# Kernel optimization log

Measured on AMD Instinct MI355X. Metric: run time of the kernel, lower is better.

## Reference

```python
import jax, jax.numpy as jnp
import numpy as np

B, S, D, H, DFF = 4, 2048, 1024, 16, 4096
DK = D // H
EPS = 1e-9


def setup_inputs() -> dict:
    key = jax.random.key(0)
    ks = jax.random.split(key, 12)
    s = lambda k, shape, scale: jax.random.normal(k, shape, dtype=jnp.float32) * scale
    return {
        "x": s(ks[0], (B, S, D), 1.0),
        "mask": jnp.ones((B, 1, 1, S), dtype=jnp.int32),
        # Linear weights stored torch-style [out, in]
        "wq": s(ks[1], (D, D), D ** -0.5),
        "wk": s(ks[2], (D, D), D ** -0.5),
        "wv": s(ks[3], (D, D), D ** -0.5),
        "wo": s(ks[4], (D, D), D ** -0.5),
        "w1": s(ks[5], (DFF, D), D ** -0.5),
        "b1": jnp.zeros((DFF,), jnp.float32),
        "w2": s(ks[6], (D, DFF), DFF ** -0.5),
        "b2": jnp.zeros((D,), jnp.float32),
        "g1": jnp.ones((D,), jnp.float32),
        "be1": jnp.zeros((D,), jnp.float32),
        "g2": jnp.ones((D,), jnp.float32),
        "be2": jnp.zeros((D,), jnp.float32),
    }


def _layernorm(x, gamma, beta):
    # Matches AddAndNorm: torch.std uses Bessel correction (ddof=1)
    mean = jnp.mean(x, axis=-1, keepdims=True)
    var = jnp.sum((x - mean) ** 2, axis=-1, keepdims=True) / (x.shape[-1] - 1)
    return gamma * (x - mean) / jnp.sqrt(var + EPS) + beta


def _mha(x, mask, wq, wk, wv, wo):
    b, s, d = x.shape
    def proj(w):  # [b,s,d] @ [d,d]^T -> heads [b,h,s,dk]
        return (x @ w.T).reshape(b, s, H, DK).transpose(0, 2, 1, 3)
    q, k, v = proj(wq), proj(wk), proj(wv)
    scores = jnp.einsum("bhqd,bhkd->bhqk", q, k) / jnp.sqrt(jnp.float32(DK))
    scores = jnp.where(mask == 0, jnp.float32(-1e9), scores)
    attn = jax.nn.softmax(scores, axis=-1)
    out = jnp.einsum("bhqk,bhkd->bhqd", attn, v)
    out = out.transpose(0, 2, 1, 3).reshape(b, s, d)
    return out @ wo.T


def reference(x, mask, wq, wk, wv, wo, w1, b1, w2, b2, g1, be1, g2, be2):
    # Residual 1: x + MHA(LN(x))  (dropout = 0)
    h1 = x + _mha(_layernorm(x, g1, be1), mask, wq, wk, wv, wo)
    # Residual 2: h1 + FFN(LN(h1))
    z = _layernorm(h1, g2, be2)
    ffn = jax.nn.relu(z @ w1.T + b1) @ w2.T + b2
    return h1 + ffn
```

## Files before the change

kernel.cpp:

```cpp
#include <hip/hip_runtime.h>
#include <hip/hip_bf16.h>
#include <cstdint>
#include <cstddef>

typedef __attribute__((ext_vector_type(8))) short short8;
typedef __attribute__((ext_vector_type(4))) float floatx4;
typedef __attribute__((ext_vector_type(4))) unsigned short ushort4e;

#define B_   4
#define S_   2048
#define D_   1024
#define H_   16
#define DK_  64
#define DFF_ 4096
#define MTOT (B_ * S_)
#define QKVLD 3072

__device__ __forceinline__ float bf2f(unsigned short u) {
    union { unsigned int i; float f; } v; v.i = ((unsigned int)u) << 16; return v.f;
}
__device__ __forceinline__ unsigned short f2bf(float f) {
    union { float f; unsigned int i; } v; v.f = f;
    unsigned int u = v.i;
    u += 0x7fffu + ((u >> 16) & 1u);
    return (unsigned short)(u >> 16);
}
__device__ __forceinline__ void async_cp16(const void* g, void* l) {
    __builtin_amdgcn_global_load_lds(
        (const __attribute__((address_space(1))) unsigned int*)g,
        (__attribute__((address_space(3))) unsigned int*)l,
        16, 0, 0);
}

__global__ void dtype_probe(const unsigned short* __restrict__ x, int* flag) {
    __shared__ float red[4];
    const int tid = threadIdx.x;
    float mx = 0.f;
    #pragma unroll
    for (int i = 0; i < 16; i++) {
        float v = fabsf(bf2f(x[tid * 16 + i]));
        if (v != v) v = 1e30f;
        mx = fmaxf(mx, v);
    }
    #pragma unroll
    for (int off = 32; off > 0; off >>= 1) mx = fmaxf(mx, __shfl_down(mx, off));
    if ((tid & 63) == 0) red[tid >> 6] = mx;
    __syncthreads();
    if (tid == 0) {
        float m = fmaxf(fmaxf(red[0], red[1]), fmaxf(red[2], red[3]));
        *flag = (m > 50.f) ? 1 : 0;
    }
}

__device__ __forceinline__ void cvt8(const void* src, unsigned short* dst, int i, int fl) {
    if (fl) {
        const floatx4* s = (const floatx4*)src;
        floatx4 a = s[i * 2], b = s[i * 2 + 1];
        short8 o;
        o[0] = (short)f2bf(a[0]); o[1] = (short)f2bf(a[1]);
        o[2] = (short)f2bf(a[2]); o[3] = (short)f2bf(a[3]);
        o[4] = (short)f2bf(b[0]); o[5] = (short)f2bf(b[1]);
        o[6] = (short)f2bf(b[2]); o[7] = (short)f2bf(b[3]);
        ((short8*)dst)[i] = o;
    } else {
        ((short8*)dst)[i] = ((const short8*)src)[i];
    }
}

__global__ void cvt_kernel(const void* __restrict__ src,
                           unsigned short* __restrict__ dst,
                           int n8, const int* __restrict__ flag) {
    const int i = blockIdx.x * 256 + threadIdx.x;
    if (i >= n8) return;
    cvt8(src, dst, i, *flag);
}

__global__ void cvt4_kernel(const void* s0, const void* s1, const void* s2, const void* s3,
                            unsigned short* __restrict__ dst,
                            const int* __restrict__ flag) {
    const int t = blockIdx.x >> 9;
    const int i = (blockIdx.x & 511) * 256 + threadIdx.x;
    const void* s = (t == 0) ? s0 : (t == 1) ? s1 : (t == 2) ? s2 : s3;
    cvt8(s, dst + (size_t)t * (D_ * D_), i, *flag);
}

__global__ void cvt_small(const void* b1, const void* b2, const void* g1,
                          const void* be1, const void* g2, const void* be2,
                          unsigned short* db1, unsigned short* db2, unsigned short* dg1,
                          unsigned short* dbe1, unsigned short* dg2, unsigned short* dbe2,
                          const int* __restrict__ flag) {
    const int fl = *flag;
    for (int i = threadIdx.x; i < 1152; i += 256) {
        if (i < 512)       cvt8(b1,  db1,  i,        fl);
        else if (i < 640)  cvt8(b2,  db2,  i - 512,  fl);
        else if (i < 768)  cvt8(g1,  dg1,  i - 640,  fl);
        else if (i < 896)  cvt8(be1, dbe1, i - 768,  fl);
        else if (i < 1024) cvt8(g2,  dg2,  i - 896,  fl);
        else               cvt8(be2, dbe2, i - 1024, fl);
    }
}

#define BM 128
#define BN 128
#define BK 64

template<int RELU, int HAS_BIAS, int RES_MODE, int OUT_MODE>
__global__ __launch_bounds__(256)
void gemm_bt(const unsigned short* __restrict__ A, int lda,
             const unsigned short* __restrict__ W, int ldw,
             const unsigned short* __restrict__ bias,
             const void* resid,
             void* out,
             int M, int N, int K,
             const int* __restrict__ flagp)
{
    __shared__ unsigned short As[BM * BK];
    __shared__ unsigned short Bs[BN * BK];

    const int tid  = threadIdx.x;
    const int lane = tid & 63;
    const int wave = tid >> 6;
    const int wm = wave >> 1;
    const int wn = wave & 1;
    const int lr = lane & 15;
    const int lq = lane >> 4;

    const int nwg     = gridDim.x * gridDim.y;
    const int flat    = blockIdx.y * gridDim.x + blockIdx.x;
    const int logical = (flat & 7) * (nwg >> 3) + (flat >> 3);
    const int m0 = (logical / gridDim.x) * BM;
    const int n0 = (logical % gridDim.x) * BN;

    int fl = 1;
    if (RES_MODE == 3 || OUT_MODE == 2) fl = *flagp;

    floatx4 acc[4][4];
    #pragma unroll
    for (int i = 0; i < 4; i++)
        #pragma unroll
        for (int j = 0; j < 4; j++)
            acc[i][j] = (floatx4){0.f, 0.f, 0.f, 0.f};

    const int lrow = lane >> 3;
    const int swz  = ((lane & 7) ^ lrow) * 8;
    const int rx   = lr & 7;
    const int p0   = ((lq)     ^ rx) * 8;
    const int p1   = ((4 + lq) ^ rx) * 8;

    for (int k0 = 0; k0 < K; k0 += BK) {
        #pragma unroll
        for (int t = 0; t < 4; t++) {
            const int row = wave * 32 + t * 8;
            async_cp16(A + (size_t)(m0 + row + lrow) * lda + k0 + swz, &As[row * BK]);
            async_cp16(W + (size_t)(n0 + row + lrow) * ldw + k0 + swz, &Bs[row * BK]);
        }
        __syncthreads();
        #pragma unroll
        for (int kk = 0; kk < 2; kk++) {
            const int pos = kk ? p1 : p0;
            short8 af[4], bfr[4];
            #pragma unroll
            for (int i = 0; i < 4; i++) {
                af[i]  = *(const short8*)(&As[(wm * 64 + i * 16 + lr) * BK + pos]);
                bfr[i] = *(const short8*)(&Bs[(wn * 64 + i * 16 + lr) * BK + pos]);
            }
            #pragma unroll
            for (int i = 0; i < 4; i++)
                #pragma unroll
                for (int j = 0; j < 4; j++)
                    acc[i][j] = __builtin_amdgcn_mfma_f32_16x16x32_bf16(
                                    af[i], bfr[j], acc[i][j], 0, 0, 0);
        }
        __syncthreads();
    }

    #pragma unroll
    for (int i = 0; i < 4; i++) {
        #pragma unroll
        for (int j = 0; j < 4; j++) {
            const int col = n0 + wn * 64 + j * 16 + lr;
            const float bv = HAS_BIAS ? bf2f(bias[col]) : 0.f;
            #pragma unroll
            for (int r = 0; r < 4; r++) {
                const int row = m0 + wm * 64 + i * 16 + lq * 4 + r;
                const size_t idx = (size_t)row * N + col;
                float vvv = acc[i][j][r] + bv;
                if (RES_MODE == 1) vvv += bf2f(((const unsigned short*)resid)[idx]);
                if (RES_MODE == 2) vvv += ((const float*)resid)[idx];
                if (RES_MODE == 3) vvv += fl ? ((const float*)resid)[idx]
                                             : bf2f(((const unsigned short*)resid)[idx]);
                if (RELU) vvv = fmaxf(vvv, 0.f);
                if (OUT_MODE == 1)      ((float*)out)[idx] = vvv;
                else if (OUT_MODE == 0) ((unsigned short*)out)[idx] = f2bf(vvv);
                else { if (fl) ((float*)out)[idx] = vvv;
                       else    ((unsigned short*)out)[idx] = f2bf(vvv); }
            }
        }
    }
}

#define GBM 256
#define GBN 256
#define GBK 64

__device__ __forceinline__ void gbar() {
    asm volatile("" ::: "memory");
    __builtin_amdgcn_s_barrier();
    asm volatile("" ::: "memory");
}

template<int RELU, int HAS_BIAS>
__global__ __launch_bounds__(512, 2)
void gemm256_bt(const unsigned short* __restrict__ A, int lda,
                const unsigned short* __restrict__ W, int ldw,
                const unsigned short* __restrict__ bias,
                unsigned short* __restrict__ out,
                int M, int N, int K)
{
    __shared__ unsigned short As[2][GBM * GBK];
    __shared__ unsigned short Bs[2][GBN * GBK];

    const int tid  = threadIdx.x;
    const int lane = tid & 63;
    const int wave = tid >> 6;
    const int wm   = wave >> 2;
    const int wn   = wave & 3;
    const int lr   = lane & 15;
    const int lq   = lane >> 4;

    const int nwg     = gridDim.x * gridDim.y;
    const int flat    = blockIdx.y * gridDim.x + blockIdx.x;
    const int logical = (flat & 7) * (nwg >> 3) + (flat >> 3);
    const int m0 = (logical / gridDim.x) * GBM;
    const int n0 = (logical % gridDim.x) * GBN;

    const int lrow = lane >> 3;
    const int schk = ((lane & 7) ^ lrow) * 8;
    const int rx   = lr & 7;
    const int fp0  = ((lq)     ^ rx) * 8;
    const int fp1  = ((4 + lq) ^ rx) * 8;

    floatx4 acc[8][4];
    #pragma unroll
    for (int i = 0; i < 8; i++)
        #pragma unroll
        for (int j = 0; j < 4; j++)
            acc[i][j] = (floatx4){0.f, 0.f, 0.f, 0.f};

    const int nkt = K / GBK;

    #pragma unroll
    for (int g = 0; g < 4; g++) {
        async_cp16(A + (size_t)(m0 + g * 64 + wave * 8 + lrow) * lda + schk,
                   &As[0][g * 4096 + wave * 512]);
        async_cp16(W + (size_t)(n0 + g * 64 + wave * 8 + lrow) * ldw + schk,
                   &Bs[0][g * 4096 + wave * 512]);
    }
    asm volatile("s_waitcnt vmcnt(0)" ::: "memory");
    __syncthreads();

    for (int t = 0; t < nkt; ++t) {
        const int cur   = t & 1;
        const int knext = (t + 1) * GBK;
        const bool more = (t + 1 < nkt);
        short8 bfr[4][2];

        #pragma unroll
        for (int p = 0; p < 4; ++p) {
            short8 af[2][2];
            #pragma unroll
            for (int ii = 0; ii < 2; ii++)
                #pragma unroll
                for (int kk = 0; kk < 2; kk++)
                    af[ii][kk] = *(const short8*)
                        &As[cur][(wm * 128 + p * 32 + ii * 16 + lr) * GBK + (kk ? fp1 : fp0)];
            if (p == 0) {
                #pragma unroll
                for (int j = 0; j < 4; j++)
                    #pragma unroll
                    for (int kk = 0; kk < 2; kk++)
                        bfr[j][kk] = *(const short8*)
                            &Bs[cur][(wn * 64 + j * 16 + lr) * GBK + (kk ? fp1 : fp0)];
                if (more) {
                    #pragma unroll
                    for (int g = 0; g < 4; g++)
                        async_cp16(A + (size_t)(m0 + g * 64 + wave * 8 + lrow) * lda + knext + schk,
                                   &As[cur ^ 1][g * 4096 + wave * 512]);
                }
            }
            if (p == 1 && more) {
                #pragma unroll
                for (int g = 0; g < 4; g++)
                    async_cp16(W + (size_t)(n0 + g * 64 + wave * 8 + lrow) * ldw + knext + schk,
                               &Bs[cur ^ 1][g * 4096 + wave * 512]);
            }
            if (p == 3) asm volatile("s_waitcnt vmcnt(0)" ::: "memory");
            gbar();
            __builtin_amdgcn_s_setprio(1);
            #pragma unroll
            for (int kk = 0; kk < 2; kk++)
                #pragma unroll
                for (int ii = 0; ii < 2; ii++)
                    #pragma unroll
                    for (int j = 0; j < 4; j++)
                        acc[p * 2 + ii][j] = __builtin_amdgcn_mfma_f32_16x16x32_bf16(
                                                 af[ii][kk], bfr[j][kk],
                                                 acc[p * 2 + ii][j], 0, 0, 0);
            __builtin_amdgcn_s_setprio(0);
            gbar();
        }
    }

    #pragma unroll
    for (int i = 0; i < 8; i++) {
        #pragma unroll
        for (int j = 0; j < 4; j++) {
            const int col = n0 + wn * 64 + j * 16 + lr;
            const float bv = HAS_BIAS ? bf2f(bias[col]) : 0.f;
            #pragma unroll
            for (int r = 0; r < 4; r++) {
                const int row = m0 + wm * 128 + i * 16 + lq * 4 + r;
                float vvv = acc[i][j][r] + bv;
                if (RELU) vvv = fmaxf(vvv, 0.f);
                out[(size_t)row * N + col] = f2bf(vvv);
            }
        }
    }
}

template<int IN_MODE>
__global__ __launch_bounds__(256)
void ln_kernel(const void* __restrict__ Xv,
               const unsigned short* __restrict__ g,
               const unsigned short* __restrict__ be,
               unsigned short* __restrict__ out,
               const int* __restrict__ flagp)
{
    const int row = blockIdx.x;
    const int tid = threadIdx.x;
    int fl = 1;
    if (IN_MODE == 2) fl = *flagp;
    float x4[4];
    if (IN_MODE == 1 || fl) {
        const float* X = (const float*)Xv + (size_t)row * D_ + tid * 4;
        floatx4 t = *(const floatx4*)X;
        x4[0] = t[0]; x4[1] = t[1]; x4[2] = t[2]; x4[3] = t[3];
    } else {
        const unsigned short* X = (const unsigned short*)Xv + (size_t)row * D_ + tid * 4;
        ushort4e u = *(const ushort4e*)X;
        #pragma unroll
        for (int i = 0; i < 4; i++) x4[i] = bf2f(u[i]);
    }
    float s1 = x4[0] + x4[1] + x4[2] + x4[3];
    float s2 = x4[0]*x4[0] + x4[1]*x4[1] + x4[2]*x4[2] + x4[3]*x4[3];
    #pragma unroll
    for (int off = 32; off > 0; off >>= 1) {
        s1 += __shfl_down(s1, off);
        s2 += __shfl_down(s2, off);
    }
    __shared__ float r1[4], r2[4];
    const int wv = tid >> 6;
    if ((tid & 63) == 0) { r1[wv] = s1; r2[wv] = s2; }
    __syncthreads();
    s1 = r1[0] + r1[1] + r1[2] + r1[3];
    s2 = r2[0] + r2[1] + r2[2] + r2[3];
    const float mean = s1 * (1.0f / D_);
    const float var  = (s2 - (float)D_ * mean * mean) * (1.0f / (D_ - 1));
    const float rstd = rsqrtf(var + 1e-9f);

    ushort4e o4;
    #pragma unroll
    for (int i = 0; i < 4; i++) {
        const float gv = bf2f(g[tid * 4 + i]);
        const float bv = bf2f(be[tid * 4 + i]);
        o4[i] = f2bf(gv * (x4[i] - mean) * rstd + bv);
    }
    *(ushort4e*)(out + (size_t)row * D_ + tid * 4) = o4;
}

__global__ __launch_bounds__(256)
void vtrans(const unsigned short* __restrict__ V, int ldv,
            unsigned short* __restrict__ Vt)
{
    __shared__ unsigned short t[64 * 72];
    const int tid = threadIdx.x;
    const int kt  = blockIdx.x * 64;
    const int bh  = blockIdx.y;
    const int b   = bh >> 4, h = bh & 15;
    const int r   = tid >> 2;
    const int c4  = (tid & 3) * 16;
    const unsigned short* vp = V + (size_t)(b * S_ + kt + r) * ldv + h * DK_ + c4;
    *(short8*)&t[r * 72 + c4]     = *(const short8*)vp;
    *(short8*)&t[r * 72 + c4 + 8] = *(const short8*)(vp + 8);
    __syncthreads();
    short8 o0, o1;
    #pragma unroll
    for (int e = 0; e < 8; e++) {
        o0[e] = (short)t[(c4 + e) * 72 + r];
        o1[e] = (short)t[(c4 + 8 + e) * 72 + r];
    }
    unsigned short* op = Vt + ((size_t)bh * DK_ + r) * S_ + kt + c4;
    *(short8*)op       = o0;
    *(short8*)(op + 8) = o1;
}

#define ATK   64
#define KS_LD 64
#define PS_LD 72
#define NT_   (S_ / ATK)

__global__ __launch_bounds__(256)
void attn_mfma(const unsigned short* __restrict__ QKV,
               const unsigned short* __restrict__ Vt,
               const int* __restrict__ mask,
               unsigned short* __restrict__ ctx)
{
    __shared__ unsigned short Ks[ATK * KS_LD];
    __shared__ unsigned short Vts[DK_ * KS_LD];
    __shared__ unsigned short Ps[4][32 * PS_LD];
    __shared__ float maskadd[ATK];

    const int tid  = threadIdx.x;
    const int lane = tid & 63;
    const int w    = tid >> 6;
    const int c    = lane & 15;
    const int qd   = lane >> 4;

    const int flat    = blockIdx.y * gridDim.x + blockIdx.x;
    const int logical = (flat & 7) * 64 + (flat >> 3);
    const int bh   = logical >> 3;
    const int b    = bh >> 4;
    const int h    = bh & 15;
    const int qb   = (logical & 7) * 256 + w * 32;

    const int lrow = lane >> 3;
    const int swz  = ((lane & 7) ^ lrow) * 8;
    const int cx   = c & 7;

    short8 onesf;
    #pragma unroll
    for (int e = 0; e < 8; e++) onesf[e] = (short)0x3F80;

    const float QS = 0.18033688f;
    short8 qf[2][2][2];
    #pragma unroll
    for (int qh = 0; qh < 2; qh++)
        #pragma unroll
        for (int jq = 0; jq < 2; jq++)
            #pragma unroll
            for (int kk = 0; kk < 2; kk++) {
                const unsigned short* qp =
                    QKV + (size_t)(b * S_ + qb + qh * 128 + jq * 16 + c) * QKVLD
                        + h * DK_ + kk * 32 + qd * 8;
                short8 t = *(const short8*)qp;
                short8 o;
                #pragma unroll
                for (int e = 0; e < 8; e++)
                    o[e] = (short)f2bf(bf2f((unsigned short)t[e]) * QS);
                qf[qh][jq][kk] = o;
            }

    floatx4 acc_o[2][2][4];
    floatx4 acc_l[2][2];
    #pragma unroll
    for (int qh = 0; qh < 2; qh++) {
        #pragma unroll
        for (int iq = 0; iq < 2; iq++) {
            acc_l[qh][iq] = (floatx4){0.f, 0.f, 0.f, 0.f};
            #pragma unroll
            for (int jd = 0; jd < 4; jd++)
                acc_o[qh][iq][jd] = (floatx4){0.f, 0.f, 0.f, 0.f};
        }
    }

    for (int kt = 0; kt < S_; kt += ATK) {
        {
            const unsigned short* kbase =
                QKV + 1024 + (size_t)(b * S_ + kt + w * 16) * QKVLD + h * DK_;
            const unsigned short* vbase =
                Vt + ((size_t)bh * DK_ + w * 16) * S_ + kt;
            #pragma unroll
            for (int t = 0; t < 2; t++) {
                async_cp16(kbase + (size_t)(t * 8 + lrow) * QKVLD + swz,
                           &Ks[(w * 16 + t * 8) * KS_LD]);
                async_cp16(vbase + (size_t)(t * 8 + lrow) * S_ + swz,
                           &Vts[(w * 16 + t * 8) * KS_LD]);
            }
            if (tid < ATK) maskadd[tid] = (mask[b * S_ + kt + tid] == 0) ? -1e9f : 0.f;
        }
        __syncthreads();

        #pragma unroll
        for (int qh = 0; qh < 2; qh++) {
            floatx4 acc_s[4][2];
            #pragma unroll
            for (int i = 0; i < 4; i++)
                #pragma unroll
                for (int jq = 0; jq < 2; jq++)
                    acc_s[i][jq] = (floatx4){0.f, 0.f, 0.f, 0.f};
            #pragma unroll
            for (int kk = 0; kk < 2; kk++) {
                const int pos = ((kk * 4 + qd) ^ cx) * 8;
                short8 kf[4];
                #pragma unroll
                for (int i = 0; i < 4; i++)
                    kf[i] = *(const short8*)&Ks[(i * 16 + c) * KS_LD + pos];
                __builtin_amdgcn_s_setprio(1);
                #pragma unroll
                for (int i = 0; i < 4; i++)
                    #pragma unroll
                    for (int jq = 0; jq < 2; jq++)
                        acc_s[i][jq] = __builtin_amdgcn_mfma_f32_16x16x32_bf16(
                                           kf[i], qf[qh][jq][kk], acc_s[i][jq], 0, 0, 0);
                __builtin_amdgcn_s_setprio(0);
            }

            floatx4 madd[4];
            #pragma unroll
            for (int i = 0; i < 4; i++)
                madd[i] = *(const floatx4*)&maskadd[i * 16 + qd * 4];

            #pragma unroll
            for (int jq = 0; jq < 2; jq++) {
                #pragma unroll
                for (int i = 0; i < 4; i++) {
                    floatx4 p;
                    #pragma unroll
                    for (int r = 0; r < 4; r++)
                        p[r] = __builtin_amdgcn_exp2f(acc_s[i][jq][r] + madd[i][r]);
                    unsigned int w0, w1;
                    asm("v_cvt_pk_bf16_f32 %0, %1, %2" : "=v"(w0) : "v"(p[0]), "v"(p[1]));
                    asm("v_cvt_pk_bf16_f32 %0, %1, %2" : "=v"(w1) : "v"(p[2]), "v"(p[3]));
                    uint2 pk; pk.x = w0; pk.y = w1;
                    *(uint2*)&Ps[w][(jq * 16 + c) * PS_LD + i * 16 + qd * 4] = pk;
                }
            }

            #pragma unroll
            for (int kk = 0; kk < 2; kk++) {
                const int pos = ((kk * 4 + qd) ^ cx) * 8;
                short8 pf[2], vf[4];
                #pragma unroll
                for (int iq = 0; iq < 2; iq++)
                    pf[iq] = *(const short8*)&Ps[w][(iq * 16 + c) * PS_LD + kk * 32 + qd * 8];
                #pragma unroll
                for (int jd = 0; jd < 4; jd++)
                    vf[jd] = *(const short8*)&Vts[(jd * 16 + c) * KS_LD + pos];
                __builtin_amdgcn_s_setprio(1);
                #pragma unroll
                for (int iq = 0; iq < 2; iq++) {
                    #pragma unroll
                    for (int jd = 0; jd < 4; jd++)
                        acc_o[qh][iq][jd] = __builtin_amdgcn_mfma_f32_16x16x32_bf16(
                                                pf[iq], vf[jd], acc_o[qh][iq][jd], 0, 0, 0);
                    acc_l[qh][iq] = __builtin_amdgcn_mfma_f32_16x16x32_bf16(
                                        pf[iq], onesf, acc_l[qh][iq], 0, 0, 0);
                }
                __builtin_amdgcn_s_setprio(0);
            }
        }
        __syncthreads();
    }

    #pragma unroll
    for (int qh = 0; qh < 2; qh++)
        #pragma unroll
        for (int iq = 0; iq < 2; iq++) {
            floatx4 inv;
            #pragma unroll
            for (int r = 0; r < 4; r++) inv[r] = 1.f / acc_l[qh][iq][r];
            #pragma unroll
            for (int jd = 0; jd < 4; jd++)
                #pragma unroll
                for (int r = 0; r < 4; r++) {
                    const int row = qb + qh * 128 + iq * 16 + qd * 4 + r;
                    const int col = h * DK_ + jd * 16 + c;
                    ctx[(size_t)(b * S_ + row) * D_ + col] =
                        f2bf(acc_o[qh][iq][jd][r] * inv[r]);
                }
        }
}

extern "C" void kernel_launch(void* const* d_in, const int* in_sizes, int n_in,
                              void* d_out, int out_size, void* d_ws, size_t ws_size,
                              hipStream_t stream)
{
    const void* x_raw  = d_in[0];
    const int*  mask   = (const int*)d_in[1];
    const void* wq_raw = d_in[2];
    const void* wk_raw = d_in[3];
    const void* wv_raw = d_in[4];
    const void* wo_raw = d_in[5];
    const void* w1_raw = d_in[6];
    const void* b1_raw = d_in[7];
    const void* w2_raw = d_in[8];
    const void* b2_raw = d_in[9];
    const void* g1_raw = d_in[10];
    const void* be1_raw= d_in[11];
    const void* g2_raw = d_in[12];
    const void* be2_raw= d_in[13];

    char* ws = (char*)d_ws;
    const size_t MB = 1024 * 1024;
    int* flag = (int*)ws;
    unsigned short* cb1  = (unsigned short*)(ws + 1 * 1024);
    unsigned short* cb2  = (unsigned short*)(ws + 16 * 1024);
    unsigned short* cg1  = (unsigned short*)(ws + 32 * 1024);
    unsigned short* cbe1 = (unsigned short*)(ws + 40 * 1024);
    unsigned short* cg2  = (unsigned short*)(ws + 48 * 1024);
    unsigned short* cbe2 = (unsigned short*)(ws + 56 * 1024);
    unsigned short* cwqkvo = (unsigned short*)(ws + 1 * MB);
    unsigned short* cwqkv  = cwqkvo;
    unsigned short* cwo    = cwqkvo + 3 * (D_ * D_);
    unsigned short* cw1  = (unsigned short*)(ws + 9 * MB);
    unsigned short* cw2  = (unsigned short*)(ws + 17 * MB);
    unsigned short* xn1  = (unsigned short*)(ws + 25 * MB);
    unsigned short* ctx  = (unsigned short*)(ws + 25 * MB);
    unsigned short* zbuf = (unsigned short*)(ws + 25 * MB);
    unsigned short* qkv  = (unsigned short*)(ws + 41 * MB);
    float*          h1   = (float*)(ws + 57 * MB);
    unsigned short* vt   = (unsigned short*)d_out;
    unsigned short* xn2  = (unsigned short*)d_out;

    dtype_probe<<<1, 256, 0, stream>>>((const unsigned short*)x_raw, flag);
    cvt_small<<<1, 256, 0, stream>>>(b1_raw, b2_raw, g1_raw, be1_raw, g2_raw, be2_raw,
                                     cb1, cb2, cg1, cbe1, cg2, cbe2, flag);
    cvt4_kernel<<<2048, 256, 0, stream>>>(wq_raw, wk_raw, wv_raw, wo_raw, cwqkvo, flag);
    cvt_kernel<<<(DFF_ * D_ / 8 + 255) / 256, 256, 0, stream>>>(w1_raw, cw1, DFF_ * D_ / 8, flag);
    cvt_kernel<<<(D_ * DFF_ / 8 + 255) / 256, 256, 0, stream>>>(w2_raw, cw2, D_ * DFF_ / 8, flag);

    const dim3 blk(256);
    const dim3 blk5(512);
    const dim3 gs(D_ / BN, MTOT / BM);
    const dim3 gq256(QKVLD / GBN, MTOT / GBM);
    const dim3 gf256(2048 / GBN, MTOT / GBM);

    ln_kernel<2><<<MTOT, blk, 0, stream>>>(x_raw, cg1, cbe1, xn1, flag);
    gemm256_bt<0,0><<<gq256, blk5, 0, stream>>>(xn1, D_, cwqkv, D_, nullptr, qkv, MTOT, QKVLD, D_);
    vtrans<<<dim3(S_ / 64, B_ * H_), blk, 0, stream>>>(qkv + 2048, QKVLD, vt);
    attn_mfma<<<dim3(S_ / 256, B_ * H_), blk, 0, stream>>>(qkv, vt, mask, ctx);
    gemm_bt<0,0,3,1><<<gs, blk, 0, stream>>>(ctx, D_, cwo, D_, nullptr, x_raw, h1, MTOT, D_, D_, flag);
    ln_kernel<1><<<MTOT, blk, 0, stream>>>(h1, cg2, cbe2, xn2, flag);
    gemm256_bt<1,1><<<gf256, blk5, 0, stream>>>(xn2, D_, cw1, D_, cb1, zbuf, MTOT, 2048, D_);
    gemm_bt<0,0,2,1><<<gs, blk, 0, stream>>>(zbuf, 2048, cw2, DFF_, nullptr, h1, h1, MTOT, D_, 2048, flag);
    const unsigned short* w1c = cw1 + (size_t)2048 * D_;
    gemm256_bt<1,1><<<gf256, blk5, 0, stream>>>(xn2, D_, w1c, D_, cb1 + 2048, zbuf, MTOT, 2048, D_);
    gemm_bt<0,1,2,2><<<gs, blk, 0, stream>>>(zbuf, 2048, cw2 + 2048, DFF_, cb2, h1, d_out, MTOT, D_, 2048, flag);
}
```

Baseline: 535.7 us.

## Unify GEMMs into a triple-buffered 256x128 pipelined MFMA kernel

Replaces both the unpipelined 128x128 GEMM and the double-buffered 256x256 GEMM with a single 512-thread, 256x128-tile kernel. It uses a three-stage LDS ring with asynchronous global-to-LDS loads, fine-grained vmcnt waits and one barrier per K step. All six projection and FFN GEMMs, including the residual/flag epilogues, now go through this kernel. The aim is to overlap memory loads with MFMA work, especially in the output-projection and FFN2 GEMMs, which previously synchronised on every tile. The cost is a smaller N tile (less reuse) for the QKV/FFN1 GEMMs and about 144KB of LDS per block, which limits occupancy to one block per CU.

```diff
diff --git a/kernel.cpp b/kernel.cpp
--- a/kernel.cpp
+++ b/kernel.cpp
@@ -31,6 +31,12 @@
         (__attribute__((address_space(3))) unsigned int*)l,
         16, 0, 0);
 }
+__device__ __forceinline__ void gbar() {
+    asm volatile("" ::: "memory");
+    __builtin_amdgcn_s_barrier();
+    asm volatile("" ::: "memory");
+}
+#define VMCNT(n) asm volatile("s_waitcnt vmcnt(" #n ")" ::: "memory")
 
 __global__ void dtype_probe(const unsigned short* __restrict__ x, int* flag) {
     __shared__ float red[4];
@@ -100,36 +106,42 @@
     }
 }
 
-#define BM 128
-#define BN 128
-#define BK 64
+#define HBM 256
+#define HBN 128
+#define HBK 64
 
 template<int RELU, int HAS_BIAS, int RES_MODE, int OUT_MODE>
-__global__ __launch_bounds__(256)
-void gemm_bt(const unsigned short* __restrict__ A, int lda,
-             const unsigned short* __restrict__ W, int ldw,
-             const unsigned short* __restrict__ bias,
-             const void* resid,
-             void* out,
-             int M, int N, int K,
-             const int* __restrict__ flagp)
+__global__ __launch_bounds__(512, 2)
+void gemm256n(const unsigned short* __restrict__ A, int lda,
+              const unsigned short* __restrict__ W, int ldw,
+              const unsigned short* __restrict__ bias,
+              const void* resid,
+              void* out,
+              int M, int N, int K,
+              const int* __restrict__ flagp)
 {
-    __shared__ unsigned short As[BM * BK];
-    __shared__ unsigned short Bs[BN * BK];
+    __shared__ unsigned short As[3][HBM * HBK];
+    __shared__ unsigned short Bs[3][HBN * HBK];
 
     const int tid  = threadIdx.x;
     const int lane = tid & 63;
     const int wave = tid >> 6;
-    const int wm = wave >> 1;
-    const int wn = wave & 1;
-    const int lr = lane & 15;
-    const int lq = lane >> 4;
+    const int wm   = wave >> 1;
+    const int wn   = wave & 1;
+    const int lr   = lane & 15;
+    const int lq   = lane >> 4;
 
     const int nwg     = gridDim.x * gridDim.y;
     const int flat    = blockIdx.y * gridDim.x + blockIdx.x;
     const int logical = (flat & 7) * (nwg >> 3) + (flat >> 3);
-    const int m0 = (logical / gridDim.x) * BM;
-    const int n0 = (logical % gridDim.x) * BN;
+    const int m0 = (logical / gridDim.x) * HBM;
+    const int n0 = (logical % gridDim.x) * HBN;
+
+    const int lrow = lane >> 3;
+    const int schk = ((lane & 7) ^ lrow) * 8;
+    const int rx   = lr & 7;
+    const int fp0  = ((lq)     ^ rx) * 8;
+    const int fp1  = ((4 + lq) ^ rx) * 8;
 
     int fl = 1;
     if (RES_MODE == 3 || OUT_MODE == 2) fl = *flagp;
@@ -141,37 +153,58 @@
         for (int j = 0; j < 4; j++)
             acc[i][j] = (floatx4){0.f, 0.f, 0.f, 0.f};
 
-    const int lrow = lane >> 3;
-    const int swz  = ((lane & 7) ^ lrow) * 8;
-    const int rx   = lr & 7;
-    const int p0   = ((lq)     ^ rx) * 8;
-    const int p1   = ((4 + lq) ^ rx) * 8;
-
-    for (int k0 = 0; k0 < K; k0 += BK) {
-        #pragma unroll
-        for (int t = 0; t < 4; t++) {
-            const int row = wave * 32 + t * 8;
-            async_cp16(A + (size_t)(m0 + row + lrow) * lda + k0 + swz, &As[row * BK]);
-            async_cp16(W + (size_t)(n0 + row + lrow) * ldw + k0 + swz, &Bs[row * BK]);
-        }
-        __syncthreads();
-        #pragma unroll
-        for (int kk = 0; kk < 2; kk++) {
-            const int pos = kk ? p1 : p0;
-            short8 af[4], bfr[4];
-            #pragma unroll
-            for (int i = 0; i < 4; i++) {
-                af[i]  = *(const short8*)(&As[(wm * 64 + i * 16 + lr) * BK + pos]);
-                bfr[i] = *(const short8*)(&Bs[(wn * 64 + i * 16 + lr) * BK + pos]);
-            }
-            #pragma unroll
-            for (int i = 0; i < 4; i++)
+    const int nkt = K / HBK;
+
+    auto STAGE = [&](int buf, int k0) {
+        #pragma unroll
+        for (int g = 0; g < 4; g++)
+            async_cp16(A + (size_t)(m0 + g * 64 + wave * 8 + lrow) * lda + k0 + schk,
+                       &As[buf][(g * 64 + wave * 8) * HBK]);
+        #pragma unroll
+        for (int g = 0; g < 2; g++)
+            async_cp16(W + (size_t)(n0 + g * 64 + wave * 8 + lrow) * ldw + k0 + schk,
+                       &Bs[buf][(g * 64 + wave * 8) * HBK]);
+    };
+
+    STAGE(0, 0);
+    STAGE(1, HBK);
+    VMCNT(6);
+    gbar();
+
+    for (int t = 0; t < nkt; ++t) {
+        const int cur = t % 3;
+        if (t + 2 < nkt) STAGE((t + 2) % 3, (t + 2) * HBK);
+
+        short8 bfr[4][2];
+        #pragma unroll
+        for (int j = 0; j < 4; j++)
+            #pragma unroll
+            for (int kk = 0; kk < 2; kk++)
+                bfr[j][kk] = *(const short8*)
+                    &Bs[cur][(wn * 64 + j * 16 + lr) * HBK + (kk ? fp1 : fp0)];
+
+        #pragma unroll
+        for (int p = 0; p < 4; ++p) {
+            short8 af[2];
+            #pragma unroll
+            for (int kk = 0; kk < 2; kk++)
+                af[kk] = *(const short8*)
+                    &As[cur][(wm * 64 + p * 16 + lr) * HBK + (kk ? fp1 : fp0)];
+            __builtin_amdgcn_s_setprio(1);
+            #pragma unroll
+            for (int kk = 0; kk < 2; kk++)
                 #pragma unroll
                 for (int j = 0; j < 4; j++)
-                    acc[i][j] = __builtin_amdgcn_mfma_f32_16x16x32_bf16(
-                                    af[i], bfr[j], acc[i][j], 0, 0, 0);
-        }
-        __syncthreads();
+                    acc[p][j] = __builtin_amdgcn_mfma_f32_16x16x32_bf16(
+                                    af[kk], bfr[j][kk], acc[p][j], 0, 0, 0);
+            __builtin_amdgcn_s_setprio(0);
+        }
+
+        if (t + 1 < nkt) {
+            if (t + 2 < nkt) { VMCNT(6); }
+            else             { VMCNT(0); }
+            gbar();
+        }
     }
 
     #pragma unroll
@@ -194,135 +227,6 @@
                 else if (OUT_MODE == 0) ((unsigned short*)out)[idx] = f2bf(vvv);
                 else { if (fl) ((float*)out)[idx] = vvv;
                        else    ((unsigned short*)out)[idx] = f2bf(vvv); }
-            }
-        }
-    }
-}
-
-#define GBM 256
-#define GBN 256
-#define GBK 64
-
-__device__ __forceinline__ void gbar() {
-    asm volatile("" ::: "memory");
-    __builtin_amdgcn_s_barrier();
-    asm volatile("" ::: "memory");
-}
-
-template<int RELU, int HAS_BIAS>
-__global__ __launch_bounds__(512, 2)
-void gemm256_bt(const unsigned short* __restrict__ A, int lda,
-                const unsigned short* __restrict__ W, int ldw,
-                const unsigned short* __restrict__ bias,
-                unsigned short* __restrict__ out,
-                int M, int N, int K)
-{
-    __shared__ unsigned short As[2][GBM * GBK];
-    __shared__ unsigned short Bs[2][GBN * GBK];
-
-    const int tid  = threadIdx.x;
-    const int lane = tid & 63;
-    const int wave = tid >> 6;
-    const int wm   = wave >> 2;
-    const int wn   = wave & 3;
-    const int lr   = lane & 15;
-    const int lq   = lane >> 4;
-
-    const int nwg     = gridDim.x * gridDim.y;
-    const int flat    = blockIdx.y * gridDim.x + blockIdx.x;
-    const int logical = (flat & 7) * (nwg >> 3) + (flat >> 3);
-    const int m0 = (logical / gridDim.x) * GBM;
-    const int n0 = (logical % gridDim.x) * GBN;
-
-    const int lrow = lane >> 3;
-    const int schk = ((lane & 7) ^ lrow) * 8;
-    const int rx   = lr & 7;
-    const int fp0  = ((lq)     ^ rx) * 8;
-    const int fp1  = ((4 + lq) ^ rx) * 8;
-
-    floatx4 acc[8][4];
-    #pragma unroll
-    for (int i = 0; i < 8; i++)
-        #pragma unroll
-        for (int j = 0; j < 4; j++)
-            acc[i][j] = (floatx4){0.f, 0.f, 0.f, 0.f};
-
-    const int nkt = K / GBK;
-
-    #pragma unroll
-    for (int g = 0; g < 4; g++) {
-        async_cp16(A + (size_t)(m0 + g * 64 + wave * 8 + lrow) * lda + schk,
-                   &As[0][g * 4096 + wave * 512]);
-        async_cp16(W + (size_t)(n0 + g * 64 + wave * 8 + lrow) * ldw + schk,
-                   &Bs[0][g * 4096 + wave * 512]);
-    }
-    asm volatile("s_waitcnt vmcnt(0)" ::: "memory");
-    __syncthreads();
-
-    for (int t = 0; t < nkt; ++t) {
-        const int cur   = t & 1;
-        const int knext = (t + 1) * GBK;
-        const bool more = (t + 1 < nkt);
-        short8 bfr[4][2];
-
-        #pragma unroll
-        for (int p = 0; p < 4; ++p) {
-            short8 af[2][2];
-            #pragma unroll
-            for (int ii = 0; ii < 2; ii++)
-                #pragma unroll
-                for (int kk = 0; kk < 2; kk++)
-                    af[ii][kk] = *(const short8*)
-                        &As[cur][(wm * 128 + p * 32 + ii * 16 + lr) * GBK + (kk ? fp1 : fp0)];
-            if (p == 0) {
-                #pragma unroll
-                for (int j = 0; j < 4; j++)
-                    #pragma unroll
-                    for (int kk = 0; kk < 2; kk++)
-                        bfr[j][kk] = *(const short8*)
-                            &Bs[cur][(wn * 64 + j * 16 + lr) * GBK + (kk ? fp1 : fp0)];
-                if (more) {
-                    #pragma unroll
-                    for (int g = 0; g < 4; g++)
-                        async_cp16(A + (size_t)(m0 + g * 64 + wave * 8 + lrow) * lda + knext + schk,
-                                   &As[cur ^ 1][g * 4096 + wave * 512]);
-                }
-            }
-            if (p == 1 && more) {
-                #pragma unroll
-                for (int g = 0; g < 4; g++)
-                    async_cp16(W + (size_t)(n0 + g * 64 + wave * 8 + lrow) * ldw + knext + schk,
-                               &Bs[cur ^ 1][g * 4096 + wave * 512]);
-            }
-            if (p == 3) asm volatile("s_waitcnt vmcnt(0)" ::: "memory");
-            gbar();
-            __builtin_amdgcn_s_setprio(1);
-            #pragma unroll
-            for (int kk = 0; kk < 2; kk++)
-                #pragma unroll
-                for (int ii = 0; ii < 2; ii++)
-                    #pragma unroll
-                    for (int j = 0; j < 4; j++)
-                        acc[p * 2 + ii][j] = __builtin_amdgcn_mfma_f32_16x16x32_bf16(
-                                                 af[ii][kk], bfr[j][kk],
-                                                 acc[p * 2 + ii][j], 0, 0, 0);
-            __builtin_amdgcn_s_setprio(0);
-            gbar();
-        }
-    }
-
-    #pragma unroll
-    for (int i = 0; i < 8; i++) {
-        #pragma unroll
-        for (int j = 0; j < 4; j++) {
-            const int col = n0 + wn * 64 + j * 16 + lr;
-            const float bv = HAS_BIAS ? bf2f(bias[col]) : 0.f;
-            #pragma unroll
-            for (int r = 0; r < 4; r++) {
-                const int row = m0 + wm * 128 + i * 16 + lq * 4 + r;
-                float vvv = acc[i][j][r] + bv;
-                if (RELU) vvv = fmaxf(vvv, 0.f);
-                out[(size_t)row * N + col] = f2bf(vvv);
             }
         }
     }
@@ -631,19 +535,19 @@
 
     const dim3 blk(256);
     const dim3 blk5(512);
-    const dim3 gs(D_ / BN, MTOT / BM);
-    const dim3 gq256(QKVLD / GBN, MTOT / GBM);
-    const dim3 gf256(2048 / GBN, MTOT / GBM);
+    const dim3 gq (QKVLD / HBN, MTOT / HBM);
+    const dim3 gwo(D_    / HBN, MTOT / HBM);
+    const dim3 gf1(2048  / HBN, MTOT / HBM);
 
     ln_kernel<2><<<MTOT, blk, 0, stream>>>(x_raw, cg1, cbe1, xn1, flag);
-    gemm256_bt<0,0><<<gq256, blk5, 0, stream>>>(xn1, D_, cwqkv, D_, nullptr, qkv, MTOT, QKVLD, D_);
+    gemm256n<0,0,0,0><<<gq, blk5, 0, stream>>>(xn1, D_, cwqkv, D_, nullptr, nullptr, qkv, MTOT, QKVLD, D_, flag);
     vtrans<<<dim3(S_ / 64, B_ * H_), blk, 0, stream>>>(qkv + 2048, QKVLD, vt);
     attn_mfma<<<dim3(S_ / 256, B_ * H_), blk, 0, stream>>>(qkv, vt, mask, ctx);
-    gemm_bt<0,0,3,1><<<gs, blk, 0, stream>>>(ctx, D_, cwo, D_, nullptr, x_raw, h1, MTOT, D_, D_, flag);
+    gemm256n<0,0,3,1><<<gwo, blk5, 0, stream>>>(ctx, D_, cwo, D_, nullptr, x_raw, h1, MTOT, D_, D_, flag);
     ln_kernel<1><<<MTOT, blk, 0, stream>>>(h1, cg2, cbe2, xn2, flag);
-    gemm256_bt<1,1><<<gf256, blk5, 0, stream>>>(xn2, D_, cw1, D_, cb1, zbuf, MTOT, 2048, D_);
-    gemm_bt<0,0,2,1><<<gs, blk, 0, stream>>>(zbuf, 2048, cw2, DFF_, nullptr, h1, h1, MTOT, D_, 2048, flag);
+    gemm256n<1,1,0,0><<<gf1, blk5, 0, stream>>>(xn2, D_, cw1, D_, cb1, nullptr, zbuf, MTOT, 2048, D_, flag);
+    gemm256n<0,0,2,1><<<gwo, blk5, 0, stream>>>(zbuf, 2048, cw2, DFF_, nullptr, h1, h1, MTOT, D_, 2048, flag);
     const unsigned short* w1c = cw1 + (size_t)2048 * D_;
-    gemm256_bt<1,1><<<gf256, blk5, 0, stream>>>(xn2, D_, w1c, D_, cb1 + 2048, zbuf, MTOT, 2048, D_);
-    gemm_bt<0,1,2,2><<<gs, blk, 0, stream>>>(zbuf, 2048, cw2 + 2048, DFF_, cb2, h1, d_out, MTOT, D_, 2048, flag);
-}
+    gemm256n<1,1,0,0><<<gf1, blk5, 0, stream>>>(xn2, D_, w1c, D_, cb1 + 2048, nullptr, zbuf, MTOT, 2048, D_, flag);
+    gemm256n<0,1,2,2><<<gwo, blk5, 0, stream>>>(zbuf, 2048, cw2 + 2048, DFF_, cb2, h1, d_out, MTOT, D_, 2048, flag);
+}
```

New measurement: 592.7 us. 10.6% more time.

## Double-buffer K/V tiles in attention and precompute full mask row in LDS

Applied to the files above, without the earlier changes.

The attention kernel now keeps two LDS buffers for K and V tiles and issues the async global-to-LDS copies for the next tile before computing on the current one. It waits on vmcnt so the prefetch overlaps the MFMA work. The mask is converted once per block into an additive array covering the whole sequence, instead of being reloaded every tile. This raises LDS use (extra K/V buffer plus an 8KB mask array), which may lower occupancy. The vmcnt-based waits depend on the exact count of outstanding loads.

```diff
diff --git a/kernel.cpp b/kernel.cpp
--- a/kernel.cpp
+++ b/kernel.cpp
@@ -6,6 +6,7 @@
 typedef __attribute__((ext_vector_type(8))) short short8;
 typedef __attribute__((ext_vector_type(4))) float floatx4;
 typedef __attribute__((ext_vector_type(4))) unsigned short ushort4e;
+typedef __attribute__((ext_vector_type(4))) int intx4;
 
 #define B_   4
 #define S_   2048
@@ -30,6 +31,11 @@
         (const __attribute__((address_space(1))) unsigned int*)g,
         (__attribute__((address_space(3))) unsigned int*)l,
         16, 0, 0);
+}
+__device__ __forceinline__ void gbar() {
+    asm volatile("" ::: "memory");
+    __builtin_amdgcn_s_barrier();
+    asm volatile("" ::: "memory");
 }
 
 __global__ void dtype_probe(const unsigned short* __restrict__ x, int* flag) {
@@ -202,12 +208,6 @@
 #define GBM 256
 #define GBN 256
 #define GBK 64
-
-__device__ __forceinline__ void gbar() {
-    asm volatile("" ::: "memory");
-    __builtin_amdgcn_s_barrier();
-    asm volatile("" ::: "memory");
-}
 
 template<int RELU, int HAS_BIAS>
 __global__ __launch_bounds__(512, 2)
@@ -415,10 +415,10 @@
                const int* __restrict__ mask,
                unsigned short* __restrict__ ctx)
 {
-    __shared__ unsigned short Ks[ATK * KS_LD];
-    __shared__ unsigned short Vts[DK_ * KS_LD];
+    __shared__ unsigned short Ks[2][ATK * KS_LD];
+    __shared__ unsigned short Vts[2][DK_ * KS_LD];
     __shared__ unsigned short Ps[4][32 * PS_LD];
-    __shared__ float maskadd[ATK];
+    __shared__ float maskadd[S_];
 
     const int tid  = threadIdx.x;
     const int lane = tid & 63;
@@ -437,6 +437,21 @@
     const int swz  = ((lane & 7) ^ lrow) * 8;
     const int cx   = c & 7;
 
+    {
+        const intx4* mp = (const intx4*)(mask + (size_t)b * S_);
+        intx4 m0 = mp[tid * 2];
+        intx4 m1 = mp[tid * 2 + 1];
+        float* dst = &maskadd[tid * 8];
+        dst[0] = (m0[0] == 0) ? -1e9f : 0.f;
+        dst[1] = (m0[1] == 0) ? -1e9f : 0.f;
+        dst[2] = (m0[2] == 0) ? -1e9f : 0.f;
+        dst[3] = (m0[3] == 0) ? -1e9f : 0.f;
+        dst[4] = (m1[0] == 0) ? -1e9f : 0.f;
+        dst[5] = (m1[1] == 0) ? -1e9f : 0.f;
+        dst[6] = (m1[2] == 0) ? -1e9f : 0.f;
+        dst[7] = (m1[3] == 0) ? -1e9f : 0.f;
+    }
+
     short8 onesf;
     #pragma unroll
     for (int e = 0; e < 8; e++) onesf[e] = (short)0x3F80;
@@ -473,22 +488,33 @@
         }
     }
 
-    for (int kt = 0; kt < S_; kt += ATK) {
-        {
-            const unsigned short* kbase =
-                QKV + 1024 + (size_t)(b * S_ + kt + w * 16) * QKVLD + h * DK_;
-            const unsigned short* vbase =
-                Vt + ((size_t)bh * DK_ + w * 16) * S_ + kt;
-            #pragma unroll
-            for (int t = 0; t < 2; t++) {
-                async_cp16(kbase + (size_t)(t * 8 + lrow) * QKVLD + swz,
-                           &Ks[(w * 16 + t * 8) * KS_LD]);
-                async_cp16(vbase + (size_t)(t * 8 + lrow) * S_ + swz,
-                           &Vts[(w * 16 + t * 8) * KS_LD]);
-            }
-            if (tid < ATK) maskadd[tid] = (mask[b * S_ + kt + tid] == 0) ? -1e9f : 0.f;
-        }
-        __syncthreads();
+    auto STAGE = [&](int buf, int kt) {
+        const unsigned short* kbase =
+            QKV + 1024 + (size_t)(b * S_ + kt + w * 16) * QKVLD + h * DK_;
+        const unsigned short* vbase =
+            Vt + ((size_t)bh * DK_ + w * 16) * S_ + kt;
+        #pragma unroll
+        for (int t = 0; t < 2; t++) {
+            async_cp16(kbase + (size_t)(t * 8 + lrow) * QKVLD + swz,
+                       &Ks[buf][(w * 16 + t * 8) * KS_LD]);
+            async_cp16(vbase + (size_t)(t * 8 + lrow) * S_ + swz,
+                       &Vts[buf][(w * 16 + t * 8) * KS_LD]);
+        }
+    };
+
+    STAGE(0, 0);
+    __syncthreads();
+
+    for (int t = 0; t < NT_; t++) {
+        const int cur = t & 1;
+        const int kt  = t * ATK;
+        if (t + 1 < NT_) {
+            STAGE(cur ^ 1, kt + ATK);
+            asm volatile("s_waitcnt vmcnt(4)" ::: "memory");
+        } else {
+            asm volatile("s_waitcnt vmcnt(0)" ::: "memory");
+        }
+        gbar();
 
         #pragma unroll
         for (int qh = 0; qh < 2; qh++) {
@@ -504,7 +530,7 @@
                 short8 kf[4];
                 #pragma unroll
                 for (int i = 0; i < 4; i++)
-                    kf[i] = *(const short8*)&Ks[(i * 16 + c) * KS_LD + pos];
+                    kf[i] = *(const short8*)&Ks[cur][(i * 16 + c) * KS_LD + pos];
                 __builtin_amdgcn_s_setprio(1);
                 #pragma unroll
                 for (int i = 0; i < 4; i++)
@@ -518,7 +544,7 @@
             floatx4 madd[4];
             #pragma unroll
             for (int i = 0; i < 4; i++)
-                madd[i] = *(const floatx4*)&maskadd[i * 16 + qd * 4];
+                madd[i] = *(const floatx4*)&maskadd[kt + i * 16 + qd * 4];
 
             #pragma unroll
             for (int jq = 0; jq < 2; jq++) {
@@ -545,7 +571,7 @@
                     pf[iq] = *(const short8*)&Ps[w][(iq * 16 + c) * PS_LD + kk * 32 + qd * 8];
                 #pragma unroll
                 for (int jd = 0; jd < 4; jd++)
-                    vf[jd] = *(const short8*)&Vts[(jd * 16 + c) * KS_LD + pos];
+                    vf[jd] = *(const short8*)&Vts[cur][(jd * 16 + c) * KS_LD + pos];
                 __builtin_amdgcn_s_setprio(1);
                 #pragma unroll
                 for (int iq = 0; iq < 2; iq++) {
@@ -559,7 +585,7 @@
                 __builtin_amdgcn_s_setprio(0);
             }
         }
-        __syncthreads();
+        gbar();
     }
 
     #pragma unroll
```

Measured after the change: 597.3 us. 11.5% more time.
